# Kernel optimization log

Hardware: AMD Instinct MI355X
Metric: run time of the kernel (lower is better)

Reference implementation:

```python
import jax, jax.numpy as jnp
import numpy as np

D, H, F, Z = 768, 12, 2048, 100   # d_model, nhead, dim_feedforward, d_z
NL = 2                            # num enc layers == num dec layers
RATIO = 0.05                      # filter_ratio
EPS = 1e-5


def _ln(x, g, b):
    m = x.mean(-1, keepdims=True)
    v = ((x - m) ** 2).mean(-1, keepdims=True)
    return (x - m) / jnp.sqrt(v + EPS) * g + b


def _mha(x, bias, qkv_w, qkv_b, out_w, out_b):
    # x: [N, L, D] (torch seq-first: seq=N responses, batch=L token positions)
    # bias: [L, N] float key-padding mask, ADDED to logits (torch float-mask semantics)
    N, L, _ = x.shape
    hd = D // H
    qkv = jnp.einsum('nld,ed->nle', x, qkv_w) + qkv_b
    q, k, v = jnp.split(qkv, 3, axis=-1)
    q = q.reshape(N, L, H, hd)
    k = k.reshape(N, L, H, hd)
    v = v.reshape(N, L, H, hd)
    scores = jnp.einsum('nlhd,mlhd->lhnm', q, k) / jnp.sqrt(jnp.float32(hd))
    scores = scores + bias[:, None, None, :]
    attn = jax.nn.softmax(scores, axis=-1)
    o = jnp.einsum('lhnm,mlhd->nlhd', attn, v).reshape(N, L, D)
    return o @ out_w.T + out_b


def _stack(x, bias, p):
    qkv_w, qkv_b, out_w, out_b, g1, b1, w1, c1, w2, c2, g2, b2 = p
    for i in range(NL):  # post-norm TransformerEncoderLayer, relu FFN, eval (no dropout)
        a = _mha(x, bias, qkv_w[i], qkv_b[i], out_w[i], out_b[i])
        x = _ln(x + a, g1[i], b1[i])
        f = jax.nn.relu(x @ w1[i].T + c1[i]) @ w2[i].T + c2[i]
        x = _ln(x + f, g2[i], b2[i])
    return x


def _anomaly_scores(emb, msk, enc_p, dec_p, pe_w, pe_b, pd_w, pd_b):
    bias = msk.T  # [L, N]
    h = _stack(emb, bias, enc_p)
    z = jnp.tanh(h @ pe_w.T + pe_b)
    zd = jnp.tanh(z @ pd_w.T + pd_b)
    d = _stack(zd, bias, dec_p)
    # per-response MSE between mean decoded and mean input embedding, summed over D
    return ((d.mean(axis=1) - emb.mean(axis=1)) ** 2).sum(-1)


def _forward(tree_lens, inputs_embeds, attention_mask, enc_p, dec_p, pe_w, pe_b, pd_w, pd_b):
    B, T, L, _ = inputs_embeds.shape
    tls = np.asarray(tree_lens)
    n_resp = tls - 1
    # pack ragged replies: rows 1..tree_len-1 of every tree -> [Ntot, L, D]
    b_idx = np.concatenate([np.full(n, b) for b, n in enumerate(n_resp)])
    t_idx = np.concatenate([np.arange(1, tl) for tl in tls])
    reply = inputs_embeds[b_idx, t_idx]
    masks = attention_mask[b_idx, t_idx]
    s = _anomaly_scores(reply, masks, enc_p, dec_p, pe_w, pe_b, pd_w, pd_b)  # [Ntot]
    Ntot = s.shape[0]
    # original: rank_idx = global_argsort filtered to indices < n_resp[b] (min is always 0)
    # == argsort of the FIRST n_resp[b] packed scores (faithful to the source's indexing)
    masked = jnp.where(jnp.arange(Ntot)[None, :] < jnp.asarray(n_resp)[:, None],
                       s[None, :], jnp.inf)
    order = jnp.argsort(masked, axis=1)[:, :T - 1]  # [B, T-1]
    n_ext = np.maximum(np.floor(n_resp * RATIO).astype(np.int64), 1)
    sel = np.arange(T - 1)[None, :] < n_ext[:, None]          # [B, T-1]
    selj = jnp.asarray(sel)
    node_idx = jnp.where(selj, order + 1, 0)                  # pad slots reuse src (node 0)
    node_full = jnp.concatenate([jnp.zeros((B, 1), node_idx.dtype), node_idx], axis=1)
    brow = jnp.arange(B)[:, None]
    new_emb = inputs_embeds[brow, node_full]                  # [B, T, L, D]
    valid = jnp.asarray(np.concatenate([np.ones((B, 1), bool), sel], axis=1)
                        ).astype(attention_mask.dtype)
    new_msk = attention_mask[brow, node_full] * valid[:, :, None]  # pad rows get zero mask
    ohidx = jnp.where(selj, order + 1, T)                     # dump masked scatters to col T
    oh = jnp.zeros((B, T + 1), jnp.int32).at[brow, ohidx].set(1)[:, :T].at[:, 0].set(1)
    ext_mask = jnp.repeat(oh[:, :, None], L, axis=2).reshape(B, T * L)
    new_tree_lens = jnp.asarray(1 + n_ext, dtype=jnp.int32)
    n_ext_adv = 0
    return oh, ext_mask, n_ext_adv, new_tree_lens, new_emb, new_msk


def setup_inputs() -> dict:
    B, T, L = 16, 32, 64
    key = jax.random.key(0)
    ks = list(jax.random.split(key, 4))
    inp = {
        'tree_lens': jax.random.randint(ks[0], (B,), T // 2, T + 1),
        'inputs_embeds': jax.random.normal(ks[1], (B, T, L, D), jnp.float32),
        'attention_mask': jnp.ones((B, T, L), jnp.float32),
    }
    kit = iter(jax.random.split(ks[2], 32))
    def w(shape):
        return jax.random.normal(next(kit), (NL,) + shape, jnp.float32) * 0.02
    for pre in ('enc', 'dec'):
        inp[pre + '_qkv_w'] = w((3 * D, D)); inp[pre + '_qkv_b'] = jnp.zeros((NL, 3 * D))
        inp[pre + '_out_w'] = w((D, D));     inp[pre + '_out_b'] = jnp.zeros((NL, D))
        inp[pre + '_ln1_g'] = jnp.ones((NL, D)); inp[pre + '_ln1_b'] = jnp.zeros((NL, D))
        inp[pre + '_w1'] = w((F, D)); inp[pre + '_c1'] = jnp.zeros((NL, F))
        inp[pre + '_w2'] = w((D, F)); inp[pre + '_c2'] = jnp.zeros((NL, D))
        inp[pre + '_ln2_g'] = jnp.ones((NL, D)); inp[pre + '_ln2_b'] = jnp.zeros((NL, D))
    inp['pe_w'] = jax.random.normal(next(kit), (Z, D), jnp.float32) * 0.02
    inp['pe_b'] = jnp.zeros((Z,), jnp.float32)
    inp['pd_w'] = jax.random.normal(next(kit), (D, Z), jnp.float32) * 0.02
    inp['pd_b'] = jnp.zeros((D,), jnp.float32)
    return inp


def reference(tree_lens, inputs_embeds, attention_mask,
              enc_qkv_w, enc_qkv_b, enc_out_w, enc_out_b, enc_ln1_g, enc_ln1_b,
              enc_w1, enc_c1, enc_w2, enc_c2, enc_ln2_g, enc_ln2_b,
              dec_qkv_w, dec_qkv_b, dec_out_w, dec_out_b, dec_ln1_g, dec_ln1_b,
              dec_w1, dec_c1, dec_w2, dec_c2, dec_ln2_g, dec_ln2_b,
              pe_w, pe_b, pd_w, pd_b):
    enc_p = (enc_qkv_w, enc_qkv_b, enc_out_w, enc_out_b, enc_ln1_g, enc_ln1_b,
             enc_w1, enc_c1, enc_w2, enc_c2, enc_ln2_g, enc_ln2_b)
    dec_p = (dec_qkv_w, dec_qkv_b, dec_out_w, dec_out_b, dec_ln1_g, dec_ln1_b,
             dec_w1, dec_c1, dec_w2, dec_c2, dec_ln2_g, dec_ln2_b)
    return _forward(tree_lens, inputs_embeds, attention_mask, enc_p, dec_p,
                    pe_w, pe_b, pd_w, pd_b)
```

## Files before the change

kernel.cpp:

```cpp
#include <hip/hip_runtime.h>
#include <hip/hip_bf16.h>
#include <math.h>


#define B_  16
#define T_  32
#define L_  64
#define D_  768
#define H_  12
#define F_  2048
#define ZR_ 100
#define ZP_ 128
#define NP_ 512
#define EPS_ 1e-5f

#define MI_NTOT  0
#define MI_NRESP 8
#define MI_OFF   32
#define MI_BIDX  64
#define MI_TIDX  576
#define MI_NODE  1088

#define WS_BIAS2 2048
#define WS_EMEAN 34816
#define WS_S     428032
#define WS_WST   428544
#define WS_BIG   1313280

#define OUT_OH   0
#define OUT_EXT  512
#define OUT_NEA  33280
#define OUT_NTL  33281
#define OUT_NEMB 33297
#define OUT_NMSK 25199121
#define OUT_XSCR 33300

typedef __attribute__((ext_vector_type(8))) short short8;
typedef __attribute__((ext_vector_type(4))) float f32x4;

__device__ inline float bf2f(unsigned s) {
  return __uint_as_float((s & 0xffffu) << 16);
}
__device__ inline unsigned short f2bf(float x) {
  unsigned u = __float_as_uint(x);
  u += 0x7fffu + ((u >> 16) & 1u);
  return (unsigned short)(u >> 16);
}
__device__ inline unsigned pack2(float a, float b) {
  return (unsigned)f2bf(a) | ((unsigned)f2bf(b) << 16);
}

__global__ void meta_kernel(const int* __restrict__ tl, int* __restrict__ mi) {
  if (threadIdx.x != 0) return;
  int off = 0;
  for (int b = 0; b < B_; b++) {
    int nr = tl[b] - 1;
    mi[MI_NRESP + b] = nr;
    mi[MI_OFF + b] = off;
    off += nr;
  }
  mi[MI_NTOT] = off;
  for (int j = 0; j < NP_; j++) {
    int b = -1, t = 0;
    if (j < off) {
      b = 0;
      while (b + 1 < B_ && j >= mi[MI_OFF + b + 1]) b++;
      t = j - mi[MI_OFF + b] + 1;
    }
    mi[MI_BIDX + j] = b;
    mi[MI_TIDX + j] = t;
  }
}

__global__ __launch_bounds__(256) void w2bf_kernel(const float* __restrict__ W,
                                                   unsigned short* __restrict__ o) {
  const int i = (blockIdx.x * 256 + threadIdx.x) * 4;
  float4 v = *(const float4*)(W + i);
  uint2 pk; pk.x = pack2(v.x, v.y); pk.y = pack2(v.z, v.w);
  *(uint2*)(o + i) = pk;
}

__global__ __launch_bounds__(192) void gather_kernel(
    const float* __restrict__ emb, const float* __restrict__ am,
    const int* __restrict__ mi, unsigned short* __restrict__ X,
    float* __restrict__ bias2) {
  const int blk = blockIdx.x;
  const int j = blk >> 6, l = blk & 63;
  const int ntot = mi[MI_NTOT];
  const int t = threadIdx.x;
  float4 v = make_float4(0.f, 0.f, 0.f, 0.f);
  if (j < ntot) {
    const int b = mi[MI_BIDX + j], tt = mi[MI_TIDX + j];
    v = ((const float4*)(emb + (size_t)((b * T_ + tt) * L_ + l) * D_))[t];
    if (t == 0) bias2[blk] = am[(b * T_ + tt) * L_ + l];
  } else {
    if (t == 0) bias2[blk] = -1e30f;
  }
  uint2 pk; pk.x = pack2(v.x, v.y); pk.y = pack2(v.z, v.w);
  *(uint2*)(X + (size_t)blk * D_ + t * 4) = pk;
}

__global__ __launch_bounds__(256) void emean_kernel(const unsigned short* __restrict__ X,
                                                    float* __restrict__ em) {
  const int j = blockIdx.x;
  int d = threadIdx.x;
  for (int c = 0; c < 3; c++, d += 256) {
    const unsigned short* p = X + (size_t)j * L_ * D_ + d;
    float s = 0.f;
    for (int l = 0; l < L_; l++) s += bf2f(p[l * D_]);
    em[j * D_ + d] = s * (1.f / 64.f);
  }
}

__device__ inline float blockSum256(float v, float* red) {
  #pragma unroll
  for (int o = 32; o > 0; o >>= 1) v += __shfl_down(v, o);
  const int lane = threadIdx.x & 63, wid = threadIdx.x >> 6;
  __syncthreads();
  if (lane == 0) red[wid] = v;
  __syncthreads();
  return red[0] + red[1] + red[2] + red[3];
}

__global__ __launch_bounds__(256) void ln_kernel(unsigned short* __restrict__ X,
                                                 const float* __restrict__ g,
                                                 const float* __restrict__ bb,
                                                 const int* __restrict__ mi) {
  const int row = blockIdx.x * 4 + (threadIdx.x >> 6);
  if (row >= mi[MI_NTOT] * L_) return;
  const int lane = threadIdx.x & 63;
  unsigned short* p = X + (size_t)row * D_;
  float v[12];
  #pragma unroll
  for (int c = 0; c < 3; c++) {
    uint2 u = *(const uint2*)(p + lane * 4 + c * 256);
    v[c * 4 + 0] = bf2f(u.x); v[c * 4 + 1] = bf2f(u.x >> 16);
    v[c * 4 + 2] = bf2f(u.y); v[c * 4 + 3] = bf2f(u.y >> 16);
  }
  float s = 0.f;
  #pragma unroll
  for (int i = 0; i < 12; i++) s += v[i];
  #pragma unroll
  for (int o = 32; o > 0; o >>= 1) s += __shfl_xor(s, o);
  const float m = s * (1.f / 768.f);
  float q = 0.f;
  #pragma unroll
  for (int i = 0; i < 12; i++) { v[i] -= m; q += v[i] * v[i]; }
  #pragma unroll
  for (int o = 32; o > 0; o >>= 1) q += __shfl_xor(q, o);
  const float r = rsqrtf(q * (1.f / 768.f) + EPS_);
  #pragma unroll
  for (int c = 0; c < 3; c++) {
    const int d = lane * 4 + c * 256;
    float4 gv = *(const float4*)(g + d);
    float4 bv = *(const float4*)(bb + d);
    uint2 pk;
    pk.x = pack2(v[c * 4 + 0] * r * gv.x + bv.x, v[c * 4 + 1] * r * gv.y + bv.y);
    pk.y = pack2(v[c * 4 + 2] * r * gv.z + bv.z, v[c * 4 + 3] * r * gv.w + bv.w);
    *(uint2*)(p + d) = pk;
  }
}

template <int ACT, bool ADD>
__global__ __launch_bounds__(256) void gemm_mfma(
    const unsigned short* __restrict__ A, int lda, int K,
    const unsigned short* __restrict__ W, int ldw,
    const float* __restrict__ bias,
    unsigned short* __restrict__ C, int ldc,
    const int* __restrict__ mi) {
  const int rows = mi[MI_NTOT] * 64;
  const int row0 = blockIdx.x * 128;
  if (row0 >= rows) return;
  const int col0 = blockIdx.y * 128;
  __shared__ unsigned short As[128 * 32];
  __shared__ unsigned short Bs[128 * 32];
  const int t = threadIdx.x;
  const int lane = t & 63, w = t >> 6;
  const int wr = w >> 1, wc = w & 1;
  const int quad = lane >> 4, l15 = lane & 15;
  f32x4 acc[4][4];
  #pragma unroll
  for (int i = 0; i < 4; i++)
    #pragma unroll
    for (int j = 0; j < 4; j++) acc[i][j] = (f32x4){0.f, 0.f, 0.f, 0.f};

  int srow[2], skg[2], schunk[2];
  #pragma unroll
  for (int r = 0; r < 2; r++) {
    const int c = r * 4 + w;
    const int g = c * 64 + lane;
    const int row = g >> 2, slot = g & 3;
    schunk[r] = c;
    srow[r] = row;
    skg[r] = slot ^ ((row >> 1) & 3);
  }
  int aoff[4], boff[4];
  #pragma unroll
  for (int m = 0; m < 4; m++) {
    const int ar = wr * 64 + m * 16 + l15;
    aoff[m] = ar * 32 + (quad ^ ((ar >> 1) & 3)) * 8;
    const int bn = wc * 64 + m * 16 + l15;
    boff[m] = bn * 32 + (quad ^ ((bn >> 1) & 3)) * 8;
  }

  for (int k0 = 0; k0 < K; k0 += 32) {
    #pragma unroll
    for (int r = 0; r < 2; r++) {
      const unsigned short* ga = A + (size_t)(row0 + srow[r]) * lda + k0 + skg[r] * 8;
      __builtin_amdgcn_global_load_lds(
          (const __attribute__((address_space(1))) void*)ga,
          (__attribute__((address_space(3))) void*)(As + schunk[r] * 512), 16, 0, 0);
      const unsigned short* gb = W + (size_t)(col0 + srow[r]) * ldw + k0 + skg[r] * 8;
      __builtin_amdgcn_global_load_lds(
          (const __attribute__((address_space(1))) void*)gb,
          (__attribute__((address_space(3))) void*)(Bs + schunk[r] * 512), 16, 0, 0);
    }
    __syncthreads();
    short8 af[4], bfr[4];
    #pragma unroll
    for (int m = 0; m < 4; m++) {
      af[m]  = *(const short8*)(As + aoff[m]);
      bfr[m] = *(const short8*)(Bs + boff[m]);
    }
    #pragma unroll
    for (int m = 0; m < 4; m++)
      #pragma unroll
      for (int n = 0; n < 4; n++)
        acc[m][n] = __builtin_amdgcn_mfma_f32_16x16x32_bf16(af[m], bfr[n], acc[m][n], 0, 0, 0);
    __syncthreads();
  }

  float bv[4];
  #pragma unroll
  for (int n = 0; n < 4; n++) bv[n] = bias[col0 + wc * 64 + n * 16 + l15];
  #pragma unroll
  for (int m = 0; m < 4; m++) {
    #pragma unroll
    for (int reg = 0; reg < 4; reg++) {
      const size_t cr = (size_t)(row0 + wr * 64 + m * 16 + quad * 4 + reg) * ldc;
      #pragma unroll
      for (int n = 0; n < 4; n++) {
        const int cn = col0 + wc * 64 + n * 16 + l15;
        float x = acc[m][n][reg] + bv[n];
        if (ACT == 1) x = fmaxf(x, 0.f);
        if (ADD) x += bf2f(C[cr + cn]);
        C[cr + cn] = f2bf(x);
      }
    }
  }
}

template <int ACT, int AT, int CT>
__global__ __launch_bounds__(256) void gemm_kernel(
    const void* __restrict__ Av, int lda, int kloop,
    const float* __restrict__ W, int kw, int nreal,
    const float* __restrict__ bias,
    void* __restrict__ Cv, int ldc,
    const int* __restrict__ mi) {
  if ((int)blockIdx.x >= mi[MI_NTOT]) return;
  __shared__ float As[16][68];
  __shared__ float Ws[16][68];
  const int t = threadIdx.x;
  const int tx = t & 15, ty = t >> 4;
  const int lrow = t >> 2, lkg = (t & 3) * 4;
  const size_t row0 = (size_t)blockIdx.x * 64;
  const int col0 = blockIdx.y * 64;
  float acc[4][4] = {};
  for (int k0 = 0; k0 < kloop; k0 += 16) {
    float a4[4];
    if (AT == 0) {
      float4 av = *(const float4*)((const float*)Av + (row0 + lrow) * (size_t)lda + k0 + lkg);
      a4[0] = av.x; a4[1] = av.y; a4[2] = av.z; a4[3] = av.w;
    } else {
      uint2 u = *(const uint2*)((const unsigned short*)Av + (row0 + lrow) * (size_t)lda + k0 + lkg);
      a4[0] = bf2f(u.x); a4[1] = bf2f(u.x >> 16);
      a4[2] = bf2f(u.y); a4[3] = bf2f(u.y >> 16);
    }
    float wv[4];
    const int wn = col0 + lrow;
    #pragma unroll
    for (int i = 0; i < 4; i++) {
      const int k = k0 + lkg + i;
      wv[i] = (wn < nreal && k < kw) ? W[(size_t)wn * kw + k] : 0.f;
    }
    __syncthreads();
    As[lkg + 0][lrow] = a4[0]; As[lkg + 1][lrow] = a4[1];
    As[lkg + 2][lrow] = a4[2]; As[lkg + 3][lrow] = a4[3];
    Ws[lkg + 0][lrow] = wv[0]; Ws[lkg + 1][lrow] = wv[1];
    Ws[lkg + 2][lrow] = wv[2]; Ws[lkg + 3][lrow] = wv[3];
    __syncthreads();
    #pragma unroll
    for (int kk = 0; kk < 16; kk++) {
      float4 av4 = *(const float4*)(&As[kk][ty * 4]);
      float4 wv4 = *(const float4*)(&Ws[kk][tx * 4]);
      float aa[4] = {av4.x, av4.y, av4.z, av4.w};
      float ww[4] = {wv4.x, wv4.y, wv4.z, wv4.w};
      #pragma unroll
      for (int i = 0; i < 4; i++)
        #pragma unroll
        for (int j = 0; j < 4; j++) acc[i][j] += aa[i] * ww[j];
    }
  }
  const int n0 = col0 + tx * 4;
  float bv[4];
  #pragma unroll
  for (int j = 0; j < 4; j++) bv[j] = (n0 + j < nreal) ? bias[n0 + j] : 0.f;
  #pragma unroll
  for (int i = 0; i < 4; i++) {
    float v[4];
    #pragma unroll
    for (int j = 0; j < 4; j++) {
      float x = acc[i][j] + bv[j];
      if (ACT == 1) x = fmaxf(x, 0.f);
      if (ACT == 2) x = tanhf(x);
      v[j] = x;
    }
    if (CT == 0) {
      float* cp = (float*)Cv + (row0 + ty * 4 + i) * (size_t)ldc + n0;
      *(float4*)cp = make_float4(v[0], v[1], v[2], v[3]);
    } else {
      unsigned short* cp = (unsigned short*)Cv + (row0 + ty * 4 + i) * (size_t)ldc + n0;
      uint2 pk; pk.x = pack2(v[0], v[1]); pk.y = pack2(v[2], v[3]);
      *(uint2*)cp = pk;
    }
  }
}

__global__ __launch_bounds__(512) void attn_kernel(
    unsigned short* __restrict__ QKV, const float* __restrict__ bias2,
    const int* __restrict__ mi) {
  const int ntot = mi[MI_NTOT];
  const int l = blockIdx.x, h = blockIdx.y;
  const int ntk = (ntot + 63) >> 6;
  __shared__ unsigned short Ks[512 * 64];
  __shared__ unsigned short Vt[8 * 4096];
  __shared__ unsigned short Ps[8][1024];
  __shared__ float bs[512];
  const int t = threadIdx.x;
  const int lane = t & 63, w = t >> 6;
  const int quad = lane >> 4, l15 = lane & 15;

  {
    const int sub = lane >> 3;
    const int cc = (lane & 7) ^ sub;
    for (int it = 0; it < ntk; it++) {
      const int m = it * 64 + w * 8 + sub;
      const unsigned short* src =
          QKV + (size_t)(m * L_ + l) * 2304 + 768 + h * 64 + cc * 8;
      __builtin_amdgcn_global_load_lds(
          (const __attribute__((address_space(1))) void*)src,
          (__attribute__((address_space(3))) void*)(Ks + it * 4096 + w * 512),
          16, 0, 0);
    }
  }
  {
    const int m = t & 63;
    const int d0 = (t >> 6) * 8;
    for (int mt = 0; mt < ntk; mt++) {
      short8 v = *(const short8*)(
          QKV + (size_t)((mt * 64 + m) * L_ + l) * 2304 + 1536 + h * 64 + d0);
      #pragma unroll
      for (int i = 0; i < 8; i++) {
        const int d = d0 + i;
        Vt[mt * 4096 + d * 64 + (((m >> 3) ^ (d & 7)) * 8) + (m & 7)] =
            (unsigned short)v[i];
      }
    }
  }
  bs[t] = bias2[t * 64 + l];
  __syncthreads();

  const int nqt = (ntot + 127) >> 7;
  for (int qt = 0; qt < nqt; qt++) {
    const int qbase = qt * 128 + w * 16;
    if (qbase >= ntot) continue;

    short8 af[2];
    #pragma unroll
    for (int kc = 0; kc < 2; kc++)
      af[kc] = *(const short8*)(
          QKV + (size_t)((qbase + l15) * L_ + l) * 2304 + h * 64 + (kc * 4 + quad) * 8);

    f32x4 oa[4];
    float runmax[4], runsum[4];
    #pragma unroll
    for (int f = 0; f < 4; f++) oa[f] = (f32x4){0.f, 0.f, 0.f, 0.f};
    #pragma unroll
    for (int r2 = 0; r2 < 4; r2++) { runmax[r2] = -3.0e38f; runsum[r2] = 0.f; }

    for (int mt = 0; mt < ntk; mt++) {
      f32x4 sv[4];
      #pragma unroll
      for (int cb = 0; cb < 4; cb++) {
        sv[cb] = (f32x4){0.f, 0.f, 0.f, 0.f};
        const int mrow = mt * 64 + cb * 16 + l15;
        #pragma unroll
        for (int kc = 0; kc < 2; kc++) {
          short8 bk = *(const short8*)(
              Ks + mrow * 64 + (((kc * 4 + quad) ^ (mrow & 7)) * 8));
          sv[cb] = __builtin_amdgcn_mfma_f32_16x16x32_bf16(af[kc], bk, sv[cb], 0, 0, 0);
        }
      }

      float bj[4];
      #pragma unroll
      for (int cb = 0; cb < 4; cb++) bj[cb] = bs[mt * 64 + cb * 16 + l15];
      float pj[4][4];
      #pragma unroll
      for (int cb = 0; cb < 4; cb++)
        #pragma unroll
        for (int r2 = 0; r2 < 4; r2++) pj[cb][r2] = sv[cb][r2] * 0.125f + bj[cb];
      float tmax[4];
      #pragma unroll
      for (int r2 = 0; r2 < 4; r2++)
        tmax[r2] = fmaxf(fmaxf(pj[0][r2], pj[1][r2]), fmaxf(pj[2][r2], pj[3][r2]));
      #pragma unroll
      for (int o2 = 1; o2 < 16; o2 <<= 1)
        #pragma unroll
        for (int r2 = 0; r2 < 4; r2++) tmax[r2] = fmaxf(tmax[r2], __shfl_xor(tmax[r2], o2));
      float tsum[4];
      #pragma unroll
      for (int r2 = 0; r2 < 4; r2++) {
        const float nmax = fmaxf(runmax[r2], tmax[r2]);
        const float alpha = __expf(runmax[r2] - nmax);
        runmax[r2] = nmax;
        float s0 = 0.f;
        #pragma unroll
        for (int cb = 0; cb < 4; cb++) { pj[cb][r2] = __expf(pj[cb][r2] - nmax); s0 += pj[cb][r2]; }
        tsum[r2] = s0;
        runsum[r2] *= alpha;
        #pragma unroll
        for (int f = 0; f < 4; f++) oa[f][r2] *= alpha;
      }
      #pragma unroll
      for (int o2 = 1; o2 < 16; o2 <<= 1)
        #pragma unroll
        for (int r2 = 0; r2 < 4; r2++) tsum[r2] += __shfl_xor(tsum[r2], o2);
      #pragma unroll
      for (int r2 = 0; r2 < 4; r2++) runsum[r2] += tsum[r2];

      #pragma unroll
      for (int cb = 0; cb < 4; cb++) {
        const int m = cb * 16 + l15;
        #pragma unroll
        for (int r2 = 0; r2 < 4; r2++) {
          const int q = quad * 4 + r2;
          Ps[w][q * 64 + (((m >> 3) ^ (q & 7)) * 8) + (m & 7)] = f2bf(pj[cb][r2]);
        }
      }
      short8 pa[2];
      #pragma unroll
      for (int kc = 0; kc < 2; kc++)
        pa[kc] = *(const short8*)(
            &Ps[w][l15 * 64 + (((kc * 4 + quad) ^ (l15 & 7)) * 8)]);
      #pragma unroll
      for (int f = 0; f < 4; f++) {
        const int d = f * 16 + l15;
        #pragma unroll
        for (int kc = 0; kc < 2; kc++) {
          short8 bv = *(const short8*)(
              Vt + mt * 4096 + d * 64 + (((kc * 4 + quad) ^ (d & 7)) * 8));
          oa[f] = __builtin_amdgcn_mfma_f32_16x16x32_bf16(pa[kc], bv, oa[f], 0, 0, 0);
        }
      }
    }

    #pragma unroll
    for (int r2 = 0; r2 < 4; r2++) {
      const float inv = 1.f / runsum[r2];
      const int q = quad * 4 + r2;
      #pragma unroll
      for (int f = 0; f < 4; f++)
        Ps[w][q * 64 + f * 16 + l15] = f2bf(oa[f][r2] * inv);
    }
    #pragma unroll
    for (int i = 0; i < 2; i++) {
      const int j = lane + i * 64;
      const int q = j >> 3, c8 = j & 7;
      short8 v = *(const short8*)(&Ps[w][j * 8]);
      *(short8*)(QKV + (size_t)((qbase + q) * L_ + l) * 2304 + h * 64 + c8 * 8) = v;
    }
  }
}

__global__ __launch_bounds__(256) void score_kernel(const unsigned short* __restrict__ X,
                                                    const float* __restrict__ em,
                                                    float* __restrict__ Sv) {
  const int j = blockIdx.x;
  const int t = threadIdx.x;
  __shared__ float red[4];
  float part = 0.f;
  for (int c = 0; c < 3; c++) {
    const int d = t + c * 256;
    const unsigned short* p = X + (size_t)j * L_ * D_ + d;
    float s = 0.f;
    for (int l = 0; l < L_; l++) s += bf2f(p[l * D_]);
    const float diff = s * (1.f / 64.f) - em[j * D_ + d];
    part += diff * diff;
  }
  const float tot = blockSum256(part, red);
  if (t == 0) Sv[j] = tot;
}

__global__ __launch_bounds__(256) void finalize_kernel(const float* __restrict__ Sv,
                                                       int* __restrict__ mi,
                                                       float* __restrict__ out) {
  const int t = threadIdx.x;
  if (t < B_) {
    const int nr = mi[MI_NRESP + t];
    float best = 3.0e38f; int bi = 0;
    for (int j = 0; j < nr; j++) {
      const float v = Sv[j];
      if (v < best) { best = v; bi = j; }
    }
    mi[MI_NODE + t] = bi + 1;
    int next = nr / 20; if (next < 1) next = 1;
    out[OUT_NTL + t] = (float)(1 + next);
  }
  if (t == 0) out[OUT_NEA] = 0.f;
  __syncthreads();
  for (int idx = t; idx < B_ * T_; idx += 256) {
    const int b = idx >> 5, tt = idx & 31;
    out[OUT_OH + idx] = (tt == 0 || tt == mi[MI_NODE + b]) ? 1.f : 0.f;
  }
}

__global__ __launch_bounds__(256) void maskout_kernel(const float* __restrict__ am,
                                                      const int* __restrict__ mi,
                                                      float* __restrict__ out) {
  const int idx = blockIdx.x * 256 + threadIdx.x;
  const int b = idx >> 11, rem = idx & 2047;
  const int tt = rem >> 6, l = rem & 63;
  const int node = mi[MI_NODE + b];
  out[OUT_EXT + idx] = (tt == 0 || tt == node) ? 1.f : 0.f;
  float nm;
  if (tt == 0)      nm = am[(b * T_) * L_ + l];
  else if (tt == 1) nm = am[(b * T_ + node) * L_ + l];
  else              nm = 0.f;
  out[OUT_NMSK + idx] = nm;
}

__global__ __launch_bounds__(192) void newemb_kernel(const float* __restrict__ emb,
                                                     const int* __restrict__ mi,
                                                     float* __restrict__ out) {
  const int blk = blockIdx.x;
  const int b = blk >> 11, rem = blk & 2047;
  const int tt = rem >> 6, l = rem & 63;
  const int srct = (tt == 1) ? mi[MI_NODE + b] : 0;
  const float4 v = ((const float4*)(emb + (size_t)((b * T_ + srct) * L_ + l) * D_))[threadIdx.x];
  float* dst = out + OUT_NEMB + (size_t)blk * D_ + threadIdx.x * 4;
  dst[0] = v.x; dst[1] = v.y; dst[2] = v.z; dst[3] = v.w;
}

extern "C" void kernel_launch(void* const* d_in, const int* in_sizes, int n_in,
                              void* d_out, int out_size, void* d_ws, size_t ws_size,
                              hipStream_t stream) {
  (void)in_sizes; (void)n_in; (void)out_size; (void)ws_size;
  const int*   tl  = (const int*)d_in[0];
  const float* emb = (const float*)d_in[1];
  const float* am  = (const float*)d_in[2];
  const float* P[28];
  for (int i = 0; i < 28; i++) P[i] = (const float*)d_in[3 + i];

  float* wsf   = (float*)d_ws;
  int*   mi    = (int*)d_ws;
  float* bias2 = wsf + WS_BIAS2;
  float* emean = wsf + WS_EMEAN;
  float* Sv    = wsf + WS_S;
  unsigned short* Wst = (unsigned short*)(wsf + WS_WST);
  unsigned short* BIG = (unsigned short*)(wsf + WS_BIG);
  float* Zb    = wsf + WS_BIG;
  float* out   = (float*)d_out;
  unsigned short* X = (unsigned short*)(out + OUT_XSCR);

  meta_kernel<<<1, 64, 0, stream>>>(tl, mi);
  gather_kernel<<<NP_ * L_, 192, 0, stream>>>(emb, am, mi, X, bias2);
  emean_kernel<<<NP_, 256, 0, stream>>>(X, emean);

  const int RT = NP_ * 64 / 128;
  const int LNB = NP_ * L_ / 4;
  for (int s = 0; s < 2; s++) {
    const float* const* q = P + s * 12;
    for (int i = 0; i < 2; i++) {
      w2bf_kernel<<<(3 * D_ * D_) / 1024, 256, 0, stream>>>(q[0] + (size_t)i * 3 * D_ * D_, Wst);
      gemm_mfma<0, false><<<dim3(RT, 18), 256, 0, stream>>>(
          X, D_, D_, Wst, D_, q[1] + i * 3 * D_, BIG, 3 * D_, mi);
      attn_kernel<<<dim3(L_, H_), 512, 0, stream>>>(BIG, bias2, mi);
      w2bf_kernel<<<(D_ * D_) / 1024, 256, 0, stream>>>(q[2] + (size_t)i * D_ * D_, Wst);
      gemm_mfma<0, true><<<dim3(RT, 6), 256, 0, stream>>>(
          BIG, 3 * D_, D_, Wst, D_, q[3] + i * D_, X, D_, mi);
      ln_kernel<<<LNB, 256, 0, stream>>>(X, q[4] + i * D_, q[5] + i * D_, mi);
      w2bf_kernel<<<(F_ * D_) / 1024, 256, 0, stream>>>(q[6] + (size_t)i * F_ * D_, Wst);
      gemm_mfma<1, false><<<dim3(RT, 16), 256, 0, stream>>>(
          X, D_, D_, Wst, D_, q[7] + i * F_, BIG, F_, mi);
      w2bf_kernel<<<(D_ * F_) / 1024, 256, 0, stream>>>(q[8] + (size_t)i * D_ * F_, Wst);
      gemm_mfma<0, true><<<dim3(RT, 6), 256, 0, stream>>>(
          BIG, F_, F_, Wst, F_, q[9] + i * D_, X, D_, mi);
      ln_kernel<<<LNB, 256, 0, stream>>>(X, q[10] + i * D_, q[11] + i * D_, mi);
    }
    if (s == 0) {
      gemm_kernel<2, 1, 0><<<dim3(NP_, 2), 256, 0, stream>>>(
          X, D_, D_, P[24], D_, ZR_, P[25], Zb, ZP_, mi);
      gemm_kernel<2, 0, 1><<<dim3(NP_, 12), 256, 0, stream>>>(
          Zb, ZP_, ZP_, P[26], ZR_, D_, P[27], X, D_, mi);
    }
  }

  score_kernel<<<NP_, 256, 0, stream>>>(X, emean, Sv);
  finalize_kernel<<<1, 256, 0, stream>>>(Sv, mi, out);
  maskout_kernel<<<128, 256, 0, stream>>>(am, mi, out);
  newemb_kernel<<<B_ * T_ * L_, 192, 0, stream>>>(emb, mi, out);
}
```

Before: 2.605 ms.

## Double-buffer LDS in MFMA GEMM and stage epilogue through LDS for vector stores

The bf16 MFMA GEMM now keeps two LDS buffers for the A and W tiles. The next K tile is loaded with global_load_lds while the current one is computed, which removes one barrier per K step and overlaps load latency with MFMA work. The epilogue writes each wave's 64x64 output tile to LDS first, then writes it out with coalesced 16-byte stores, and the residual add is done on 8-element vectors. The cost is more LDS use, which may lower occupancy. In the ADD path the result is now rounded to bf16 twice, before and after the residual is added, which slightly changes numerics.

```diff
diff --git a/kernel.cpp b/kernel.cpp
--- a/kernel.cpp
+++ b/kernel.cpp
@@ -172,8 +172,7 @@
   const int row0 = blockIdx.x * 128;
   if (row0 >= rows) return;
   const int col0 = blockIdx.y * 128;
-  __shared__ unsigned short As[128 * 32];
-  __shared__ unsigned short Bs[128 * 32];
+  __shared__ unsigned short Sh[4][4096];
   const int t = threadIdx.x;
   const int lane = t & 63, w = t >> 6;
   const int wr = w >> 1, wc = w & 1;
@@ -184,15 +183,18 @@
     #pragma unroll
     for (int j = 0; j < 4; j++) acc[i][j] = (f32x4){0.f, 0.f, 0.f, 0.f};
 
-  int srow[2], skg[2], schunk[2];
+  int schunk[2];
+  const unsigned short* gA[2];
+  const unsigned short* gB[2];
   #pragma unroll
   for (int r = 0; r < 2; r++) {
     const int c = r * 4 + w;
     const int g = c * 64 + lane;
     const int row = g >> 2, slot = g & 3;
+    const int kg = slot ^ ((row >> 1) & 3);
     schunk[r] = c;
-    srow[r] = row;
-    skg[r] = slot ^ ((row >> 1) & 3);
+    gA[r] = A + (size_t)(row0 + row) * lda + kg * 8;
+    gB[r] = W + (size_t)(col0 + row) * ldw + kg * 8;
   }
   int aoff[4], boff[4];
   #pragma unroll
@@ -203,33 +205,50 @@
     boff[m] = bn * 32 + (quad ^ ((bn >> 1) & 3)) * 8;
   }
 
-  for (int k0 = 0; k0 < K; k0 += 32) {
-    #pragma unroll
-    for (int r = 0; r < 2; r++) {
-      const unsigned short* ga = A + (size_t)(row0 + srow[r]) * lda + k0 + skg[r] * 8;
-      __builtin_amdgcn_global_load_lds(
-          (const __attribute__((address_space(1))) void*)ga,
-          (__attribute__((address_space(3))) void*)(As + schunk[r] * 512), 16, 0, 0);
-      const unsigned short* gb = W + (size_t)(col0 + srow[r]) * ldw + k0 + skg[r] * 8;
-      __builtin_amdgcn_global_load_lds(
-          (const __attribute__((address_space(1))) void*)gb,
-          (__attribute__((address_space(3))) void*)(Bs + schunk[r] * 512), 16, 0, 0);
-    }
+#define STAGE_(bi, kk)                                                         \
+  for (int r = 0; r < 2; r++) {                                                \
+    __builtin_amdgcn_global_load_lds(                                          \
+        (const __attribute__((address_space(1))) void*)(gA[r] + (kk)),         \
+        (__attribute__((address_space(3))) void*)(Sh[bi] + schunk[r] * 512),   \
+        16, 0, 0);                                                             \
+    __builtin_amdgcn_global_load_lds(                                          \
+        (const __attribute__((address_space(1))) void*)(gB[r] + (kk)),         \
+        (__attribute__((address_space(3))) void*)(Sh[2 + (bi)] + schunk[r] * 512), \
+        16, 0, 0);                                                             \
+  }
+
+#define COMPUTE_(bi)                                                           \
+  {                                                                            \
+    short8 af[4], bfr[4];                                                      \
+    _Pragma("unroll")                                                          \
+    for (int m = 0; m < 4; m++) {                                              \
+      af[m]  = *(const short8*)(Sh[bi] + aoff[m]);                             \
+      bfr[m] = *(const short8*)(Sh[2 + (bi)] + boff[m]);                       \
+    }                                                                          \
+    _Pragma("unroll")                                                          \
+    for (int m = 0; m < 4; m++)                                                \
+      _Pragma("unroll")                                                        \
+      for (int n = 0; n < 4; n++)                                              \
+        acc[m][n] = __builtin_amdgcn_mfma_f32_16x16x32_bf16(af[m], bfr[n],     \
+                                                            acc[m][n], 0, 0, 0); \
+  }
+
+  STAGE_(0, 0);
+  __syncthreads();
+  int cur = 0;
+  for (int k0 = 32; k0 < K; k0 += 32) {
+    STAGE_(cur ^ 1, k0);
+    COMPUTE_(cur);
     __syncthreads();
-    short8 af[4], bfr[4];
-    #pragma unroll
-    for (int m = 0; m < 4; m++) {
-      af[m]  = *(const short8*)(As + aoff[m]);
-      bfr[m] = *(const short8*)(Bs + boff[m]);
-    }
-    #pragma unroll
-    for (int m = 0; m < 4; m++)
-      #pragma unroll
-      for (int n = 0; n < 4; n++)
-        acc[m][n] = __builtin_amdgcn_mfma_f32_16x16x32_bf16(af[m], bfr[n], acc[m][n], 0, 0, 0);
-    __syncthreads();
-  }
-
+    cur ^= 1;
+  }
+  COMPUTE_(cur);
+  __syncthreads();
+
+#undef STAGE_
+#undef COMPUTE_
+
+  unsigned short* slice = &Sh[0][0] + w * 4096;
   float bv[4];
   #pragma unroll
   for (int n = 0; n < 4; n++) bv[n] = bias[col0 + wc * 64 + n * 16 + l15];
@@ -237,16 +256,30 @@
   for (int m = 0; m < 4; m++) {
     #pragma unroll
     for (int reg = 0; reg < 4; reg++) {
-      const size_t cr = (size_t)(row0 + wr * 64 + m * 16 + quad * 4 + reg) * ldc;
+      const int r64 = m * 16 + quad * 4 + reg;
       #pragma unroll
       for (int n = 0; n < 4; n++) {
-        const int cn = col0 + wc * 64 + n * 16 + l15;
         float x = acc[m][n][reg] + bv[n];
         if (ACT == 1) x = fmaxf(x, 0.f);
-        if (ADD) x += bf2f(C[cr + cn]);
-        C[cr + cn] = f2bf(x);
+        slice[r64 * 64 + n * 16 + l15] = f2bf(x);
       }
     }
+  }
+  unsigned short* crow = C + (size_t)(row0 + wr * 64) * ldc + col0 + wc * 64;
+  #pragma unroll
+  for (int i = 0; i < 8; i++) {
+    const int j = i * 64 + lane;
+    const int r64 = j >> 3, c8 = (j & 7) * 8;
+    short8 v = *(const short8*)(slice + j * 8);
+    unsigned short* cp = crow + (size_t)r64 * ldc + c8;
+    if (ADD) {
+      short8 cv = *(const short8*)cp;
+      #pragma unroll
+      for (int e = 0; e < 8; e++)
+        v[e] = (short)f2bf(bf2f((unsigned short)v[e]) +
+                           bf2f((unsigned short)cv[e]));
+    }
+    *(short8*)cp = v;
   }
 }
 
```

Measured after the change: 2.488 ms. 4.5% less time.
